# Optimization experiments

Hardware: AMD Instinct MI355X
Metric: run time of the kernel (lower is better)

## Reference

```python
import jax, jax.numpy as jnp
import numpy as np

# init config (from init_kwargs)
NUM_ANCHORS = 5
NUM_CLASSES = 80
ANCHORS = jnp.array([[0.57273, 0.677385], [1.87446, 2.06253], [3.33843, 5.47434],
                     [7.88282, 3.52778], [9.77052, 9.16828]], dtype=jnp.float32)
MAX_BOXES = 50  # hard-coded loop bound in build_targets


def setup_inputs() -> dict:
    key = jax.random.key(0)
    k1, k2 = jax.random.split(key)
    output = jax.random.normal(k1, (64, 425, 38, 38), dtype=jnp.float32)
    # target: (nB, 50*5) of [cls, cx, cy, w, h] normalized to (0,1); strictly
    # positive entries -> all 50 boxes valid (original loop breaks at first 0).
    target = jax.random.uniform(k2, (64, 250), dtype=jnp.float32, minval=0.02, maxval=0.98)
    return {"output": output, "target": target, "reqd_class_index": 14}


def _cls_mask(target, nH, nW):
    """Vectorized build_targets: only cls_mask affects the returned loss.
    For each valid GT box, best anchor = argmax IoU of (0,0,aw,ah) vs (0,0,gw,gh)
    (first max wins, matching the strict > in the Python loop); mark cell
    (b, best_n, gj, gi)."""
    nB = target.shape[0]
    tgt = target.reshape(nB, MAX_BOXES, 5)
    # loop breaks at first t with target[b][5t+1]==0 -> cumulative validity
    valid = jnp.cumprod((tgt[:, :, 1] != 0).astype(jnp.int32), axis=1) > 0
    gx = tgt[:, :, 1] * nW
    gy = tgt[:, :, 2] * nH
    gw = tgt[:, :, 3] * nW  # (nB, T)
    gh = tgt[:, :, 4] * nH
    gi = jnp.clip(jnp.floor(gx).astype(jnp.int32), 0, nW - 1)
    gj = jnp.clip(jnp.floor(gy).astype(jnp.int32), 0, nH - 1)
    aw, ah = ANCHORS[:, 0], ANCHORS[:, 1]  # (nA,)
    # centered-box IoU: intersection widths are min of the widths
    inter = jnp.minimum(gw[..., None], aw) * jnp.minimum(gh[..., None], ah)  # (nB,T,nA)
    iou = inter / (gw[..., None] * gh[..., None] + aw * ah - inter)
    best_n = jnp.argmax(iou, axis=-1).astype(jnp.int32)  # (nB, T), first-max tiebreak
    b = jnp.arange(nB, dtype=jnp.int32)[:, None]
    flat = ((b * NUM_ANCHORS + best_n) * nH + gj) * nW + gi  # (nB, T)
    n_cells = nB * NUM_ANCHORS * nH * nW
    mask = jnp.zeros((n_cells,), jnp.int32).at[flat.ravel()].max(valid.ravel().astype(jnp.int32))
    return mask > 0


def reference(output, target, reqd_class_index):
    nB, _, nH, nW = output.shape
    out = output.reshape(nB, NUM_ANCHORS, 5 + NUM_CLASSES, nH, nW)
    # class logits -> (nB, nA, nH, nW, nC), matching torch's
    # view(nB*nA, nC, nH*nW).transpose(1,2).view(-1, nC) flattening order
    cls_logits = jnp.transpose(out[:, :, 5:, :, :], (0, 1, 3, 4, 2))
    probs = jax.nn.softmax(cls_logits, axis=-1)
    p = probs[..., reqd_class_index].reshape(-1)  # prob of required class per cell
    mask = _cls_mask(target, nH, nW)
    m = mask.astype(p.dtype)
    # L1Loss(cls_prob2, 0, size_average=True) over selected cells == masked mean
    loss = jnp.sum(p * m) / jnp.sum(m)
    max_class_prob = jnp.max(jnp.where(mask, p, -jnp.inf))
    return loss, max_class_prob
```

## Files before the change

kernel.cpp:

```cpp
#include <hip/hip_runtime.h>
#include <stdint.h>
#include <math.h>

#define NUM_ANCHORS 5
#define NUM_CLASSES 80
#define MAX_BOXES   50


__global__ void init_ws(uint32_t* ws, int n_words) {
    int i = blockIdx.x * blockDim.x + threadIdx.x;
    if (i < n_words) ws[i] = (i == 2) ? 0xFF800000u : 0u;
}

__global__ void build_list(const float* __restrict__ target,
                           uint32_t* __restrict__ hdr,
                           int* __restrict__ list,
                           uint32_t* __restrict__ bm,
                           int nH, int nW) {
#pragma clang fp contract(off)
    int b = blockIdx.x;
    int lane = threadIdx.x;
    const float* t = target + (long)b * MAX_BOXES * 5;
    float x = 1.0f, y = 0.0f, w = 0.0f, h = 0.0f;
    if (lane < MAX_BOXES) {
        x = t[lane * 5 + 1];
        y = t[lane * 5 + 2];
        w = t[lane * 5 + 3];
        h = t[lane * 5 + 4];
    }
    unsigned long long zb = __ballot(lane < MAX_BOXES && x == 0.0f);
    int first_zero = zb ? (__ffsll(zb) - 1) : MAX_BOXES;
    if (lane >= first_zero) return;

    float gx = x * (float)nW;
    float gy = y * (float)nH;
    float gw = w * (float)nW;
    float gh = h * (float)nH;
    int gi = min(max((int)floorf(gx), 0), nW - 1);
    int gj = min(max((int)floorf(gy), 0), nH - 1);

    const float aw[NUM_ANCHORS] = {0.57273f, 1.87446f, 3.33843f, 7.88282f, 9.77052f};
    const float ah[NUM_ANCHORS] = {0.677385f, 2.06253f, 5.47434f, 3.52778f, 9.16828f};
    int best = 0; float bestiou = -1.0f;
    #pragma unroll
    for (int n = 0; n < NUM_ANCHORS; ++n) {
        float inter = fminf(gw, aw[n]) * fminf(gh, ah[n]);
        float uni   = gw * gh + aw[n] * ah[n] - inter;
        float iou   = inter / uni;
        if (iou > bestiou) { bestiou = iou; best = n; }
    }
    int flat = ((b * NUM_ANCHORS + best) * nH + gj) * nW + gi;
    uint32_t bit = 1u << (flat & 31);
    uint32_t old = atomicOr(&bm[flat >> 5], bit);
    if (!(old & bit)) {
        int idx = (int)atomicAdd(&hdr[1], 1u);
        list[idx] = flat;
    }
}

__global__ void __launch_bounds__(256)
reduce_list(const float* __restrict__ output,
            const uint32_t* __restrict__ hdr,
            const int* __restrict__ list,
            float* __restrict__ sumf,
            int* __restrict__ maxbits,
            const int* __restrict__ reqd,
            int HW) {
    __shared__ float sp[4];
    __shared__ float sm[4];
    int lane = threadIdx.x & 63;
    int wave = threadIdx.x >> 6;
    int g = blockIdx.x * 4 + wave;
    int count = (int)hdr[1];
    float p = 0.0f, pm = -INFINITY;
    if (g < count) {
        int cell = list[g];
        int ba = cell / HW;
        int hw = cell - ba * HW;
        const float* ptr = output + ((long)(ba * (5 + NUM_CLASSES) + 5)) * HW + hw;
        float v0 = ptr[(long)lane * HW];
        float v1 = (lane < NUM_CLASSES - 64) ? ptr[(long)(lane + 64) * HW] : -INFINITY;
        float mx = fmaxf(v0, v1);
        #pragma unroll
        for (int off = 32; off; off >>= 1) mx = fmaxf(mx, __shfl_xor(mx, off, 64));
        float e0 = expf(v0 - mx);
        float e1 = (lane < NUM_CLASSES - 64) ? expf(v1 - mx) : 0.0f;
        float s = e0 + e1;
        #pragma unroll
        for (int off = 32; off; off >>= 1) s += __shfl_xor(s, off, 64);
        int rq = *reqd;
        float lr = (rq < 64) ? __shfl(v0, rq, 64) : __shfl(v1, rq - 64, 64);
        p = expf(lr - mx) / s;
        pm = p;
    }
    if (lane == 0) { sp[wave] = p; sm[wave] = pm; }
    __syncthreads();
    if (threadIdx.x == 0) {
        float ts = 0.0f, tm = -INFINITY;
        #pragma unroll
        for (int w = 0; w < 4; ++w) { ts += sp[w]; tm = fmaxf(tm, sm[w]); }
        if (tm > -INFINITY) {
            atomicAdd(sumf, ts);
            atomicMax(maxbits, __float_as_int(tm));
        }
    }
}

__global__ void finalize(const float* __restrict__ sumf,
                         const uint32_t* __restrict__ hdr,
                         const int* __restrict__ maxbits,
                         float* __restrict__ out) {
    out[0] = sumf[0] / (float)hdr[1];
    out[1] = __int_as_float(maxbits[0]);
}

extern "C" void kernel_launch(void* const* d_in, const int* in_sizes, int n_in,
                              void* d_out, int out_size, void* d_ws, size_t ws_size,
                              hipStream_t stream) {
    const float* output = (const float*)d_in[0];
    const float* target = (const float*)d_in[1];
    const int*   reqd   = (const int*)d_in[2];
    float* out = (float*)d_out;

    int nB = in_sizes[1] / (MAX_BOXES * 5);
    int HW = in_sizes[0] / (nB * (5 + NUM_CLASSES) * NUM_ANCHORS);
    int nW = 1; while (nW * nW < HW) ++nW;
    int nH = HW / nW;
    long cells = (long)nB * NUM_ANCHORS * nH * nW;

    int listCap = nB * MAX_BOXES;
    int bmWords = (int)((cells + 31) / 32);
    int n_words = 4 + listCap + bmWords;

    uint32_t* ws   = (uint32_t*)d_ws;
    uint32_t* hdr  = ws;
    float*    sumf = (float*)ws;
    int*      maxb = (int*)(ws + 2);
    int*      list = (int*)(ws + 4);
    uint32_t* bm   = ws + 4 + listCap;

    init_ws<<<(n_words + 255) / 256, 256, 0, stream>>>(ws, n_words);

    build_list<<<nB, 64, 0, stream>>>(target, hdr, list, bm, nH, nW);

    int rblocks = (listCap + 3) / 4;
    reduce_list<<<rblocks, 256, 0, stream>>>(output, hdr, list, sumf, maxb,
                                             reqd, HW);

    finalize<<<1, 1, 0, stream>>>(sumf, hdr, maxb, out);
}
```

Baseline: 215.3 us.

## Fuse workspace init into build_list, dedup in-wave, finalize via last-block ticket

Drops the separate init kernel and the big bitmap by zeroing only four header words inside a single-block build_list. Duplicate cells are now detected within each wave using shuffles instead of an atomic bitmap, which is valid because a cell index includes the batch and each wave handles one batch. The finalize kernel is removed: the last reduce block to finish, found with an atomic done counter, writes the outputs. This cuts launches from four to two and avoids clearing the bitmap, but build_list now runs on a single block and loops over the batches.

```diff
diff --git a/kernel.cpp b/kernel.cpp
--- a/kernel.cpp
+++ b/kernel.cpp
@@ -7,71 +7,82 @@
 #define MAX_BOXES   50
 
 
-__global__ void init_ws(uint32_t* ws, int n_words) {
-    int i = blockIdx.x * blockDim.x + threadIdx.x;
-    if (i < n_words) ws[i] = (i == 2) ? 0xFF800000u : 0u;
-}
+__global__ void __launch_bounds__(1024)
+build_list(const float* __restrict__ target,
+           uint32_t* __restrict__ ws,
+           int nB, int nH, int nW) {
+#pragma clang fp contract(off)
+    int tid = threadIdx.x;
+    if (tid < 4) ws[tid] = (tid == 2) ? 0xFF800000u : 0u;
+    __syncthreads();
 
-__global__ void build_list(const float* __restrict__ target,
-                           uint32_t* __restrict__ hdr,
-                           int* __restrict__ list,
-                           uint32_t* __restrict__ bm,
-                           int nH, int nW) {
-#pragma clang fp contract(off)
-    int b = blockIdx.x;
-    int lane = threadIdx.x;
-    const float* t = target + (long)b * MAX_BOXES * 5;
-    float x = 1.0f, y = 0.0f, w = 0.0f, h = 0.0f;
-    if (lane < MAX_BOXES) {
-        x = t[lane * 5 + 1];
-        y = t[lane * 5 + 2];
-        w = t[lane * 5 + 3];
-        h = t[lane * 5 + 4];
-    }
-    unsigned long long zb = __ballot(lane < MAX_BOXES && x == 0.0f);
-    int first_zero = zb ? (__ffsll(zb) - 1) : MAX_BOXES;
-    if (lane >= first_zero) return;
+    int lane  = tid & 63;
+    int wave  = tid >> 6;
+    int nWav  = blockDim.x >> 6;
+    int* list = (int*)(ws + 4);
 
-    float gx = x * (float)nW;
-    float gy = y * (float)nH;
-    float gw = w * (float)nW;
-    float gh = h * (float)nH;
-    int gi = min(max((int)floorf(gx), 0), nW - 1);
-    int gj = min(max((int)floorf(gy), 0), nH - 1);
+    for (int b = wave; b < nB; b += nWav) {
+        const float* t = target + (long)b * MAX_BOXES * 5;
+        float x = 1.0f, y = 0.0f, w = 0.0f, h = 0.0f;
+        if (lane < MAX_BOXES) {
+            x = t[lane * 5 + 1];
+            y = t[lane * 5 + 2];
+            w = t[lane * 5 + 3];
+            h = t[lane * 5 + 4];
+        }
+        unsigned long long zb = __ballot(lane < MAX_BOXES && x == 0.0f);
+        int first_zero = zb ? (__ffsll(zb) - 1) : MAX_BOXES;
+        bool valid = lane < first_zero;
 
-    const float aw[NUM_ANCHORS] = {0.57273f, 1.87446f, 3.33843f, 7.88282f, 9.77052f};
-    const float ah[NUM_ANCHORS] = {0.677385f, 2.06253f, 5.47434f, 3.52778f, 9.16828f};
-    int best = 0; float bestiou = -1.0f;
-    #pragma unroll
-    for (int n = 0; n < NUM_ANCHORS; ++n) {
-        float inter = fminf(gw, aw[n]) * fminf(gh, ah[n]);
-        float uni   = gw * gh + aw[n] * ah[n] - inter;
-        float iou   = inter / uni;
-        if (iou > bestiou) { bestiou = iou; best = n; }
-    }
-    int flat = ((b * NUM_ANCHORS + best) * nH + gj) * nW + gi;
-    uint32_t bit = 1u << (flat & 31);
-    uint32_t old = atomicOr(&bm[flat >> 5], bit);
-    if (!(old & bit)) {
-        int idx = (int)atomicAdd(&hdr[1], 1u);
-        list[idx] = flat;
+        float gx = x * (float)nW;
+        float gy = y * (float)nH;
+        float gw = w * (float)nW;
+        float gh = h * (float)nH;
+        int gi = min(max((int)floorf(gx), 0), nW - 1);
+        int gj = min(max((int)floorf(gy), 0), nH - 1);
+
+        const float aw[NUM_ANCHORS] = {0.57273f, 1.87446f, 3.33843f, 7.88282f, 9.77052f};
+        const float ah[NUM_ANCHORS] = {0.677385f, 2.06253f, 5.47434f, 3.52778f, 9.16828f};
+        int best = 0; float bestiou = -1.0f;
+        #pragma unroll
+        for (int n = 0; n < NUM_ANCHORS; ++n) {
+            float inter = fminf(gw, aw[n]) * fminf(gh, ah[n]);
+            float uni   = gw * gh + aw[n] * ah[n] - inter;
+            float iou   = inter / uni;
+            if (iou > bestiou) { bestiou = iou; best = n; }
+        }
+        int flat = ((b * NUM_ANCHORS + best) * nH + gj) * nW + gi;
+
+        unsigned long long vmask = __ballot(valid);
+        bool dup = false;
+        for (int j = 0; j < MAX_BOXES; ++j) {
+            int fj = __shfl(flat, j, 64);
+            dup |= (j < lane) && (((vmask >> j) & 1ull) != 0) && (fj == flat);
+        }
+        if (valid && !dup) {
+            int idx = (int)atomicAdd(&ws[1], 1u);
+            list[idx] = flat;
+        }
     }
 }
 
 __global__ void __launch_bounds__(256)
 reduce_list(const float* __restrict__ output,
-            const uint32_t* __restrict__ hdr,
-            const int* __restrict__ list,
-            float* __restrict__ sumf,
-            int* __restrict__ maxbits,
+            uint32_t* __restrict__ ws,
             const int* __restrict__ reqd,
+            float* __restrict__ out,
             int HW) {
     __shared__ float sp[4];
     __shared__ float sm[4];
+    float*    sumf    = (float*)ws;
+    int*      maxbits = (int*)(ws + 2);
+    uint32_t* done    = ws + 3;
+    const int* list   = (const int*)(ws + 4);
+
     int lane = threadIdx.x & 63;
     int wave = threadIdx.x >> 6;
     int g = blockIdx.x * 4 + wave;
-    int count = (int)hdr[1];
+    int count = (int)ws[1];
     float p = 0.0f, pm = -INFINITY;
     if (g < count) {
         int cell = list[g];
@@ -103,15 +114,15 @@
             atomicAdd(sumf, ts);
             atomicMax(maxbits, __float_as_int(tm));
         }
+        __threadfence();
+        uint32_t old = atomicAdd(done, 1u);
+        if (old == (uint32_t)gridDim.x - 1u) {
+            float ts2 = atomicAdd(sumf, 0.0f);
+            int   tm2 = atomicMax(maxbits, (int)0x80000000);
+            out[0] = ts2 / (float)count;
+            out[1] = __int_as_float(tm2);
+        }
     }
-}
-
-__global__ void finalize(const float* __restrict__ sumf,
-                         const uint32_t* __restrict__ hdr,
-                         const int* __restrict__ maxbits,
-                         float* __restrict__ out) {
-    out[0] = sumf[0] / (float)hdr[1];
-    out[1] = __int_as_float(maxbits[0]);
 }
 
 extern "C" void kernel_launch(void* const* d_in, const int* in_sizes, int n_in,
@@ -126,26 +137,12 @@
     int HW = in_sizes[0] / (nB * (5 + NUM_CLASSES) * NUM_ANCHORS);
     int nW = 1; while (nW * nW < HW) ++nW;
     int nH = HW / nW;
-    long cells = (long)nB * NUM_ANCHORS * nH * nW;
+
+    uint32_t* ws = (uint32_t*)d_ws;
+
+    build_list<<<1, 1024, 0, stream>>>(target, ws, nB, nH, nW);
 
     int listCap = nB * MAX_BOXES;
-    int bmWords = (int)((cells + 31) / 32);
-    int n_words = 4 + listCap + bmWords;
-
-    uint32_t* ws   = (uint32_t*)d_ws;
-    uint32_t* hdr  = ws;
-    float*    sumf = (float*)ws;
-    int*      maxb = (int*)(ws + 2);
-    int*      list = (int*)(ws + 4);
-    uint32_t* bm   = ws + 4 + listCap;
-
-    init_ws<<<(n_words + 255) / 256, 256, 0, stream>>>(ws, n_words);
-
-    build_list<<<nB, 64, 0, stream>>>(target, hdr, list, bm, nH, nW);
-
     int rblocks = (listCap + 3) / 4;
-    reduce_list<<<rblocks, 256, 0, stream>>>(output, hdr, list, sumf, maxb,
-                                             reqd, HW);
-
-    finalize<<<1, 1, 0, stream>>>(sumf, hdr, maxb, out);
+    reduce_list<<<rblocks, 256, 0, stream>>>(output, ws, reqd, out, HW);
 }
```

Result: slower. 241.7 us (+12.3%).
